# Performance work log

Measured on AMD Instinct MI355X. Metric: run time of the kernel, lower is better.

## Reference

```python
import jax, jax.numpy as jnp
import numpy as np

D = 2048          # input_size
B_NECK = 512      # bottleneck_size
NUM_LANGS = 16
ZETA = 1.1
GAMMA = -0.1
LN_EPS = 1e-5


def setup_inputs() -> dict:
    key = jax.random.key(0)
    ks = jax.random.split(key, 8)
    x = jax.random.normal(ks[0], (8, 2048, D), dtype=jnp.float32)
    # xavier_uniform for linear weights
    lim_d = float(np.sqrt(6.0 / (D + B_NECK)))
    down_w = jax.random.uniform(ks[1], (B_NECK, D), minval=-lim_d, maxval=lim_d, dtype=jnp.float32)
    up_w = jax.random.uniform(ks[2], (D, B_NECK), minval=-lim_d, maxval=lim_d, dtype=jnp.float32)
    down_b = jnp.zeros((B_NECK,), dtype=jnp.float32)
    up_b = jnp.zeros((D,), dtype=jnp.float32)
    ln_g = jnp.ones((D,), dtype=jnp.float32)
    ln_b = jnp.zeros((D,), dtype=jnp.float32)
    down_loga = 0.01 * jax.random.normal(ks[3], (NUM_LANGS, D), dtype=jnp.float32)
    up_loga = 0.01 * jax.random.normal(ks[4], (NUM_LANGS, B_NECK), dtype=jnp.float32)
    return {"x": x, "down_w": down_w, "down_b": down_b, "up_w": up_w,
            "up_b": up_b, "ln_g": ln_g, "ln_b": ln_b,
            "down_loga": down_loga, "up_loga": up_loga, "lang_id": 3}


def _det_mask(loga_row):
    # eval-mode L0 gate: hardtanh(sigmoid(loga)*(zeta-gamma)+gamma, 0, 1)
    return jnp.clip(jax.nn.sigmoid(loga_row) * (ZETA - GAMMA) + GAMMA, 0.0, 1.0)


def reference(x, down_w, down_b, up_w, up_b, ln_g, ln_b, down_loga, up_loga, lang_id):
    shortcut = x
    # LayerNorm over last dim
    mu = jnp.mean(x, axis=-1, keepdims=True)
    var = jnp.mean(jnp.square(x - mu), axis=-1, keepdims=True)
    h = (x - mu) * jax.lax.rsqrt(var + LN_EPS) * ln_g + ln_b
    # down projection with per-input-feature gate (mask scales weight columns)
    dmask = _det_mask(down_loga[lang_id])            # [D]
    h = jnp.einsum('bsd,kd->bsk', h * dmask, down_w) + down_b  # [B,S,B_NECK]
    h = jax.nn.relu(h)
    # up projection with per-bottleneck gate
    umask = _det_mask(up_loga[lang_id])              # [B_NECK]
    h = jnp.einsum('bsk,dk->bsd', h * umask, up_w) + up_b       # [B,S,D]
    return h + shortcut
```

## Files before the change

kernel.cpp:

```cpp
#include <hip/hip_runtime.h>
#include <cstdint>
#include <cstddef>

typedef unsigned short u16;
typedef __attribute__((ext_vector_type(4))) float f32x4;
typedef __attribute__((ext_vector_type(8))) short bf16x8;

#define LN_EPS 1e-5f

__device__ __forceinline__ u16 f2bf(float f) {
  unsigned int u = __float_as_uint(f);
  u += 0x7FFFu + ((u >> 16) & 1u);
  return (u16)(u >> 16);
}

__device__ __forceinline__ float l0gate(float loga) {
  float s = 1.0f / (1.0f + expf(-loga));
  float v = s * 1.2f - 0.1f;
  return fminf(fmaxf(v, 0.0f), 1.0f);
}

__device__ __forceinline__ void llds16(u16* lds, const u16* g) {
  __builtin_amdgcn_global_load_lds(
      (const __attribute__((address_space(1))) unsigned int*)g,
      (__attribute__((address_space(3))) unsigned int*)lds, 16, 0, 0);
}

__global__ __launch_bounds__(256) void prep_weights(
    const float* __restrict__ dw, const float* __restrict__ uw,
    const float* __restrict__ dloga, const float* __restrict__ uloga,
    const int* __restrict__ lang,
    u16* __restrict__ dwb, u16* __restrict__ uwb) {
  const int lid = lang[0];
  const unsigned i = blockIdx.x * 256u + threadIdx.x;
  dwb[i] = f2bf(dw[i] * l0gate(dloga[lid * 2048 + (i & 2047u)]));
  uwb[i] = f2bf(uw[i] * l0gate(uloga[lid * 512 + (i & 511u)]));
}

__global__ __launch_bounds__(256) void ln_kernel(
    const float* __restrict__ x, const float* __restrict__ g,
    const float* __restrict__ b, u16* __restrict__ h1) {
  const int row = blockIdx.x;
  const int tid = threadIdx.x;
  const float4* xr = (const float4*)(x + (size_t)row * 2048);
  float4 v0 = xr[tid * 2 + 0];
  float4 v1 = xr[tid * 2 + 1];
  float s = v0.x + v0.y + v0.z + v0.w + v1.x + v1.y + v1.z + v1.w;
  float q = v0.x * v0.x + v0.y * v0.y + v0.z * v0.z + v0.w * v0.w +
            v1.x * v1.x + v1.y * v1.y + v1.z * v1.z + v1.w * v1.w;
#pragma unroll
  for (int off = 32; off > 0; off >>= 1) {
    s += __shfl_down(s, off, 64);
    q += __shfl_down(q, off, 64);
  }
  __shared__ float ss[4], sq[4], sstat[2];
  const int wave = tid >> 6, lane = tid & 63;
  if (lane == 0) { ss[wave] = s; sq[wave] = q; }
  __syncthreads();
  if (tid == 0) {
    float S = ss[0] + ss[1] + ss[2] + ss[3];
    float Q = sq[0] + sq[1] + sq[2] + sq[3];
    float mu = S * (1.0f / 2048.0f);
    float var = Q * (1.0f / 2048.0f) - mu * mu;
    sstat[0] = mu;
    sstat[1] = rsqrtf(var + LN_EPS);
  }
  __syncthreads();
  const float mu = sstat[0], rs = sstat[1];
  const float4* g4 = (const float4*)g;
  const float4* b4 = (const float4*)b;
  float4 ga = g4[tid * 2], gb = g4[tid * 2 + 1];
  float4 ba = b4[tid * 2], bb = b4[tid * 2 + 1];
  union { u16 us[8]; uint4 u; } p;
  p.us[0] = f2bf((v0.x - mu) * rs * ga.x + ba.x);
  p.us[1] = f2bf((v0.y - mu) * rs * ga.y + ba.y);
  p.us[2] = f2bf((v0.z - mu) * rs * ga.z + ba.z);
  p.us[3] = f2bf((v0.w - mu) * rs * ga.w + ba.w);
  p.us[4] = f2bf((v1.x - mu) * rs * gb.x + bb.x);
  p.us[5] = f2bf((v1.y - mu) * rs * gb.y + bb.y);
  p.us[6] = f2bf((v1.z - mu) * rs * gb.z + bb.z);
  p.us[7] = f2bf((v1.w - mu) * rs * gb.w + bb.w);
  ((uint4*)(h1 + (size_t)row * 2048))[tid] = p.u;
}

template <int EPI>
__global__ __launch_bounds__(256) void gemm_bt(
    const u16* __restrict__ A, const u16* __restrict__ B,
    int M, int N, int K, int NX,
    const float* __restrict__ bias,
    const float* __restrict__ resid,
    void* __restrict__ outp) {
  __shared__ __align__(16) char smem[65536];
  u16* As = (u16*)smem;
  u16* Bs = (u16*)(smem + 32768);
  float* Cs = (float*)smem;

  const int tid = threadIdx.x;
  const int wave = tid >> 6, lane = tid & 63;
  const int wr = (wave >> 1) * 64;
  const int wc = (wave & 1) * 64;
  const int lrow = lane & 15, lk = lane >> 4;

  const int nwg = gridDim.x;
  const int wg = (blockIdx.x & 7) * (nwg >> 3) + (blockIdx.x >> 3);
  const int bx = wg % NX, by = wg / NX;
  const size_t m0 = (size_t)by * 128;
  const size_t n0 = (size_t)bx * 128;

  f32x4 acc[4][4] = {};

  const int srow = lane >> 3;
  const int sslot = (lane & 7) ^ ((lane >> 3) & 7);
  auto STAGE = [&](int buf, int k0) {
#pragma unroll
    for (int c = 0; c < 4; ++c) {
      const int seg = c * 4 + wave;
      const int r = seg * 8 + srow;
      llds16(As + buf * 8192 + seg * 512, A + (m0 + r) * (size_t)K + (k0 + sslot * 8));
      llds16(Bs + buf * 8192 + seg * 512, B + (n0 + r) * (size_t)K + (k0 + sslot * 8));
    }
  };

  const int NT = K >> 6;
  STAGE(0, 0);

  for (int t = 0; t < NT; ++t) {
    const int cur = t & 1;
    if (t + 1 < NT) {
      STAGE(cur ^ 1, (t + 1) << 6);
      asm volatile("s_waitcnt vmcnt(8)" ::: "memory");
    } else {
      asm volatile("s_waitcnt vmcnt(0)" ::: "memory");
    }
    __builtin_amdgcn_s_barrier();
    asm volatile("" ::: "memory");

    const u16* Ab = As + cur * 8192;
    const u16* Bb = Bs + cur * 8192;
#pragma unroll
    for (int ks = 0; ks < 2; ++ks) {
      bf16x8 af[4], bfr[4];
#pragma unroll
      for (int m = 0; m < 4; ++m)
        af[m] = *(const bf16x8*)&Ab[(wr + m * 16 + lrow) * 64 +
                                    ((unsigned)(ks * 4 + lk) ^ (lane & 7)) * 8];
#pragma unroll
      for (int n = 0; n < 4; ++n)
        bfr[n] = *(const bf16x8*)&Bb[(wc + n * 16 + lrow) * 64 +
                                     ((unsigned)(ks * 4 + lk) ^ (lane & 7)) * 8];
      __builtin_amdgcn_s_setprio(1);
#pragma unroll
      for (int m = 0; m < 4; ++m)
#pragma unroll
        for (int n = 0; n < 4; ++n)
          acc[m][n] = __builtin_amdgcn_mfma_f32_16x16x32_bf16(af[m], bfr[n],
                                                              acc[m][n], 0, 0, 0);
      __builtin_amdgcn_s_setprio(0);
    }
    asm volatile("s_waitcnt lgkmcnt(0)" ::: "memory");
    __builtin_amdgcn_s_barrier();
    asm volatile("" ::: "memory");
  }

  float4 rsd[16];
  if (EPI == 2) {
#pragma unroll
    for (int j = 0; j < 16; ++j) {
      const int flat = tid * 4 + j * 1024;
      const int row = flat >> 7, col = flat & 127;
      rsd[j] = *(const float4*)&resid[(m0 + row) * (size_t)N + n0 + col];
    }
  }

#pragma unroll
  for (int n = 0; n < 4; ++n) {
    const int col = wc + n * 16 + lrow;
    const float bv = bias[n0 + col];
#pragma unroll
    for (int m = 0; m < 4; ++m) {
#pragma unroll
      for (int r = 0; r < 4; ++r) {
        const int row = wr + m * 16 + lk * 4 + r;
        Cs[row * 128 + ((col + ((row >> 2) << 3)) & 127)] = acc[m][n][r] + bv;
      }
    }
  }
  asm volatile("s_waitcnt lgkmcnt(0)" ::: "memory");
  __builtin_amdgcn_s_barrier();
  asm volatile("" ::: "memory");

  if (EPI == 2) {
#pragma unroll
    for (int j = 0; j < 16; ++j) {
      const int flat = tid * 4 + j * 1024;
      const int row = flat >> 7, col = flat & 127;
      const float4 c = *(const float4*)&Cs[row * 128 + ((col + ((row >> 2) << 3)) & 127)];
      float4 o;
      o.x = c.x + rsd[j].x; o.y = c.y + rsd[j].y;
      o.z = c.z + rsd[j].z; o.w = c.w + rsd[j].w;
      *(float4*)&((float*)outp)[(m0 + row) * (size_t)N + n0 + col] = o;
    }
  } else {
#pragma unroll
    for (int j = 0; j < 8; ++j) {
      const int flat = tid * 8 + j * 2048;
      const int row = flat >> 7, col = flat & 127;
      const int cp = (col + ((row >> 2) << 3)) & 127;
      const float4 c0 = *(const float4*)&Cs[row * 128 + cp];
      const float4 c1 = *(const float4*)&Cs[row * 128 + cp + 4];
      union { u16 us[8]; uint4 u; } p;
      p.us[0] = f2bf(fmaxf(c0.x, 0.0f)); p.us[1] = f2bf(fmaxf(c0.y, 0.0f));
      p.us[2] = f2bf(fmaxf(c0.z, 0.0f)); p.us[3] = f2bf(fmaxf(c0.w, 0.0f));
      p.us[4] = f2bf(fmaxf(c1.x, 0.0f)); p.us[5] = f2bf(fmaxf(c1.y, 0.0f));
      p.us[6] = f2bf(fmaxf(c1.z, 0.0f)); p.us[7] = f2bf(fmaxf(c1.w, 0.0f));
      *(uint4*)&((u16*)outp)[(m0 + row) * (size_t)N + n0 + col] = p.u;
    }
  }
}

extern "C" void kernel_launch(void* const* d_in, const int* in_sizes, int n_in,
                              void* d_out, int out_size, void* d_ws, size_t ws_size,
                              hipStream_t stream) {
  const float* x         = (const float*)d_in[0];
  const float* down_w    = (const float*)d_in[1];
  const float* down_b    = (const float*)d_in[2];
  const float* up_w      = (const float*)d_in[3];
  const float* up_b      = (const float*)d_in[4];
  const float* ln_g      = (const float*)d_in[5];
  const float* ln_b      = (const float*)d_in[6];
  const float* down_loga = (const float*)d_in[7];
  const float* up_loga   = (const float*)d_in[8];
  const int*   lang      = (const int*)d_in[9];

  const int D = 2048, BNK = 512;
  const int M = in_sizes[0] / D;

  char* ws = (char*)d_ws;
  u16* h1  = (u16*)ws;
  u16* h2  = (u16*)(ws + (size_t)M * D * 2);
  u16* dwb = (u16*)(ws + (size_t)M * D * 2 + (size_t)M * BNK * 2);
  u16* uwb = dwb + (size_t)BNK * D;

  prep_weights<<<(BNK * D) / 256, 256, 0, stream>>>(down_w, up_w, down_loga,
                                                    up_loga, lang, dwb, uwb);
  ln_kernel<<<M, 256, 0, stream>>>(x, ln_g, ln_b, h1);
  const int nwg1 = (BNK / 128) * (M / 128);
  const int nwg2 = (D / 128) * (M / 128);
  gemm_bt<1><<<nwg1, 256, 0, stream>>>(h1, dwb, M, BNK, D, BNK / 128,
                                       down_b, nullptr, h2);
  gemm_bt<2><<<nwg2, 256, 0, stream>>>(h2, uwb, M, D, BNK, D / 128,
                                       up_b, x, d_out);
}
```

Before: 153.1 us.

## Shrink GEMM tiles to 128x64 with K-step 32 and raise occupancy

Changes the GEMM workgroup tile from 128x128 with a K-step of 64 to 128x64 with a K-step of 32. This halves shared memory to 32KB and requests 4 workgroups per CU through launch bounds, aiming for more occupancy and more workgroups across the CUs. The LDS XOR swizzle on the fragment reads is dropped, which may cause bank conflicts. Each tile also gets less reuse per load, and the shorter K-step doubles the number of barrier iterations.

```diff
diff --git a/kernel.cpp b/kernel.cpp
--- a/kernel.cpp
+++ b/kernel.cpp
@@ -84,104 +84,101 @@
 }
 
 template <int EPI>
-__global__ __launch_bounds__(256) void gemm_bt(
+__global__ __launch_bounds__(256, 4) void gemm_bt(
     const u16* __restrict__ A, const u16* __restrict__ B,
     int M, int N, int K, int NX,
     const float* __restrict__ bias,
     const float* __restrict__ resid,
     void* __restrict__ outp) {
-  __shared__ __align__(16) char smem[65536];
+  __shared__ __align__(16) char smem[32768];
   u16* As = (u16*)smem;
-  u16* Bs = (u16*)(smem + 32768);
+  u16* Bs = (u16*)(smem + 16384);
   float* Cs = (float*)smem;
 
   const int tid = threadIdx.x;
   const int wave = tid >> 6, lane = tid & 63;
   const int wr = (wave >> 1) * 64;
-  const int wc = (wave & 1) * 64;
+  const int wcc = (wave & 1) * 32;
   const int lrow = lane & 15, lk = lane >> 4;
 
   const int nwg = gridDim.x;
   const int wg = (blockIdx.x & 7) * (nwg >> 3) + (blockIdx.x >> 3);
   const int bx = wg % NX, by = wg / NX;
   const size_t m0 = (size_t)by * 128;
-  const size_t n0 = (size_t)bx * 128;
-
-  f32x4 acc[4][4] = {};
-
-  const int srow = lane >> 3;
-  const int sslot = (lane & 7) ^ ((lane >> 3) & 7);
+  const size_t n0 = (size_t)bx * 64;
+
+  f32x4 acc[4][2] = {};
+
+  const int crow = lane >> 2;
+  const int ckk = (lane & 3) * 8;
   auto STAGE = [&](int buf, int k0) {
 #pragma unroll
-    for (int c = 0; c < 4; ++c) {
-      const int seg = c * 4 + wave;
-      const int r = seg * 8 + srow;
-      llds16(As + buf * 8192 + seg * 512, A + (m0 + r) * (size_t)K + (k0 + sslot * 8));
-      llds16(Bs + buf * 8192 + seg * 512, B + (n0 + r) * (size_t)K + (k0 + sslot * 8));
-    }
+    for (int c = 0; c < 2; ++c) {
+      const int q = wave * 2 + c;
+      llds16(As + buf * 4096 + q * 512,
+             A + (m0 + q * 16 + crow) * (size_t)K + (k0 + ckk));
+    }
+    llds16(Bs + buf * 2048 + wave * 512,
+           B + (n0 + wave * 16 + crow) * (size_t)K + (k0 + ckk));
   };
 
-  const int NT = K >> 6;
+  const int NT = K >> 5;
   STAGE(0, 0);
 
   for (int t = 0; t < NT; ++t) {
     const int cur = t & 1;
     if (t + 1 < NT) {
-      STAGE(cur ^ 1, (t + 1) << 6);
-      asm volatile("s_waitcnt vmcnt(8)" ::: "memory");
+      STAGE(cur ^ 1, (t + 1) << 5);
+      asm volatile("s_waitcnt vmcnt(3)" ::: "memory");
     } else {
       asm volatile("s_waitcnt vmcnt(0)" ::: "memory");
     }
     __builtin_amdgcn_s_barrier();
     asm volatile("" ::: "memory");
 
-    const u16* Ab = As + cur * 8192;
-    const u16* Bb = Bs + cur * 8192;
-#pragma unroll
-    for (int ks = 0; ks < 2; ++ks) {
-      bf16x8 af[4], bfr[4];
-#pragma unroll
-      for (int m = 0; m < 4; ++m)
-        af[m] = *(const bf16x8*)&Ab[(wr + m * 16 + lrow) * 64 +
-                                    ((unsigned)(ks * 4 + lk) ^ (lane & 7)) * 8];
-#pragma unroll
-      for (int n = 0; n < 4; ++n)
-        bfr[n] = *(const bf16x8*)&Bb[(wc + n * 16 + lrow) * 64 +
-                                     ((unsigned)(ks * 4 + lk) ^ (lane & 7)) * 8];
-      __builtin_amdgcn_s_setprio(1);
-#pragma unroll
-      for (int m = 0; m < 4; ++m)
-#pragma unroll
-        for (int n = 0; n < 4; ++n)
-          acc[m][n] = __builtin_amdgcn_mfma_f32_16x16x32_bf16(af[m], bfr[n],
-                                                              acc[m][n], 0, 0, 0);
-      __builtin_amdgcn_s_setprio(0);
-    }
+    const u16* Ab = As + cur * 4096;
+    const u16* Bb = Bs + cur * 2048;
+    bf16x8 af[4], bfr[2];
+#pragma unroll
+    for (int m = 0; m < 4; ++m)
+      af[m] = *(const bf16x8*)&Ab[(wr + m * 16 + lrow) * 32 + lk * 8];
+#pragma unroll
+    for (int n = 0; n < 2; ++n)
+      bfr[n] = *(const bf16x8*)&Bb[(wcc + n * 16 + lrow) * 32 + lk * 8];
+    __builtin_amdgcn_s_setprio(1);
+#pragma unroll
+    for (int m = 0; m < 4; ++m)
+#pragma unroll
+      for (int n = 0; n < 2; ++n)
+        acc[m][n] = __builtin_amdgcn_mfma_f32_16x16x32_bf16(af[m], bfr[n],
+                                                            acc[m][n], 0, 0, 0);
+    __builtin_amdgcn_s_setprio(0);
+
     asm volatile("s_waitcnt lgkmcnt(0)" ::: "memory");
     __builtin_amdgcn_s_barrier();
     asm volatile("" ::: "memory");
   }
 
-  float4 rsd[16];
+  float4 rsd[8];
   if (EPI == 2) {
 #pragma unroll
-    for (int j = 0; j < 16; ++j) {
+    for (int j = 0; j < 8; ++j) {
       const int flat = tid * 4 + j * 1024;
-      const int row = flat >> 7, col = flat & 127;
-      rsd[j] = *(const float4*)&resid[(m0 + row) * (size_t)N + n0 + col];
-    }
-  }
-
-#pragma unroll
-  for (int n = 0; n < 4; ++n) {
-    const int col = wc + n * 16 + lrow;
-    const float bv = bias[n0 + col];
+      const int row = flat >> 6, c = flat & 63;
+      rsd[j] = *(const float4*)&resid[(m0 + row) * (size_t)N + n0 + c];
+    }
+  }
+
+#pragma unroll
+  for (int n = 0; n < 2; ++n) {
+    const int c = wcc + n * 16 + lrow;
+    const float bv = bias[n0 + c];
 #pragma unroll
     for (int m = 0; m < 4; ++m) {
 #pragma unroll
       for (int r = 0; r < 4; ++r) {
         const int row = wr + m * 16 + lk * 4 + r;
-        Cs[row * 128 + ((col + ((row >> 2) << 3)) & 127)] = acc[m][n][r] + bv;
+        Cs[row * 64 + ((c + ((row >> 2) << 3)) & 63)] = acc[m][n][r] + bv;
       }
     }
   }
@@ -191,29 +188,29 @@
 
   if (EPI == 2) {
 #pragma unroll
-    for (int j = 0; j < 16; ++j) {
+    for (int j = 0; j < 8; ++j) {
       const int flat = tid * 4 + j * 1024;
-      const int row = flat >> 7, col = flat & 127;
-      const float4 c = *(const float4*)&Cs[row * 128 + ((col + ((row >> 2) << 3)) & 127)];
+      const int row = flat >> 6, c = flat & 63;
+      const float4 cc = *(const float4*)&Cs[row * 64 + ((c + ((row >> 2) << 3)) & 63)];
       float4 o;
-      o.x = c.x + rsd[j].x; o.y = c.y + rsd[j].y;
-      o.z = c.z + rsd[j].z; o.w = c.w + rsd[j].w;
-      *(float4*)&((float*)outp)[(m0 + row) * (size_t)N + n0 + col] = o;
+      o.x = cc.x + rsd[j].x; o.y = cc.y + rsd[j].y;
+      o.z = cc.z + rsd[j].z; o.w = cc.w + rsd[j].w;
+      *(float4*)&((float*)outp)[(m0 + row) * (size_t)N + n0 + c] = o;
     }
   } else {
 #pragma unroll
-    for (int j = 0; j < 8; ++j) {
+    for (int j = 0; j < 4; ++j) {
       const int flat = tid * 8 + j * 2048;
-      const int row = flat >> 7, col = flat & 127;
-      const int cp = (col + ((row >> 2) << 3)) & 127;
-      const float4 c0 = *(const float4*)&Cs[row * 128 + cp];
-      const float4 c1 = *(const float4*)&Cs[row * 128 + cp + 4];
+      const int row = flat >> 6, c = flat & 63;
+      const int cp = (c + ((row >> 2) << 3)) & 63;
+      const float4 c0 = *(const float4*)&Cs[row * 64 + cp];
+      const float4 c1 = *(const float4*)&Cs[row * 64 + cp + 4];
       union { u16 us[8]; uint4 u; } p;
       p.us[0] = f2bf(fmaxf(c0.x, 0.0f)); p.us[1] = f2bf(fmaxf(c0.y, 0.0f));
       p.us[2] = f2bf(fmaxf(c0.z, 0.0f)); p.us[3] = f2bf(fmaxf(c0.w, 0.0f));
       p.us[4] = f2bf(fmaxf(c1.x, 0.0f)); p.us[5] = f2bf(fmaxf(c1.y, 0.0f));
       p.us[6] = f2bf(fmaxf(c1.z, 0.0f)); p.us[7] = f2bf(fmaxf(c1.w, 0.0f));
-      *(uint4*)&((u16*)outp)[(m0 + row) * (size_t)N + n0 + col] = p.u;
+      *(uint4*)&((u16*)outp)[(m0 + row) * (size_t)N + n0 + c] = p.u;
     }
   }
 }
@@ -244,10 +241,10 @@
   prep_weights<<<(BNK * D) / 256, 256, 0, stream>>>(down_w, up_w, down_loga,
                                                     up_loga, lang, dwb, uwb);
   ln_kernel<<<M, 256, 0, stream>>>(x, ln_g, ln_b, h1);
-  const int nwg1 = (BNK / 128) * (M / 128);
-  const int nwg2 = (D / 128) * (M / 128);
-  gemm_bt<1><<<nwg1, 256, 0, stream>>>(h1, dwb, M, BNK, D, BNK / 128,
+  const int nwg1 = (BNK / 64) * (M / 128);
+  const int nwg2 = (D / 64) * (M / 128);
+  gemm_bt<1><<<nwg1, 256, 0, stream>>>(h1, dwb, M, BNK, D, BNK / 64,
                                        down_b, nullptr, h2);
-  gemm_bt<2><<<nwg2, 256, 0, stream>>>(h2, uwb, M, D, BNK, D / 128,
+  gemm_bt<2><<<nwg2, 256, 0, stream>>>(h2, uwb, M, D, BNK, D / 64,
                                        up_b, x, d_out);
 }
```

New measurement: 180.1 us. 17.6% more time.

## Fold LayerNorm into down-projection GEMM via algebraic mean/scale correction

Applied to the files above, without the earlier changes.

Removes the separate LayerNorm kernel and its bf16 intermediate. The down GEMM now reads raw fp32 x, converts it to bf16 in registers while accumulating per-row sums and sums of squares, and applies the normalisation in the epilogue as rs*(acc - mu*u) + w. The gain is folded into the weights, and a new prep kernel computes u and w from the weights, beta and bias. The up GEMM also prefetches the residual during its K loop. The risk is precision, since un-normalised x is rounded to bf16 and the mean is subtracted after accumulation, which can cause cancellation. Each down-GEMM block also rereads x, once per output column tile.

```diff
diff --git a/kernel.cpp b/kernel.cpp
--- a/kernel.cpp
+++ b/kernel.cpp
@@ -29,111 +29,112 @@
 __global__ __launch_bounds__(256) void prep_weights(
     const float* __restrict__ dw, const float* __restrict__ uw,
     const float* __restrict__ dloga, const float* __restrict__ uloga,
-    const int* __restrict__ lang,
+    const int* __restrict__ lang, const float* __restrict__ g,
     u16* __restrict__ dwb, u16* __restrict__ uwb) {
   const int lid = lang[0];
   const unsigned i = blockIdx.x * 256u + threadIdx.x;
-  dwb[i] = f2bf(dw[i] * l0gate(dloga[lid * 2048 + (i & 2047u)]));
+  dwb[i] = f2bf(dw[i] * l0gate(dloga[lid * 2048 + (i & 2047u)]) * g[i & 2047u]);
   uwb[i] = f2bf(uw[i] * l0gate(uloga[lid * 512 + (i & 511u)]));
 }
 
-__global__ __launch_bounds__(256) void ln_kernel(
-    const float* __restrict__ x, const float* __restrict__ g,
-    const float* __restrict__ b, u16* __restrict__ h1) {
-  const int row = blockIdx.x;
-  const int tid = threadIdx.x;
-  const float4* xr = (const float4*)(x + (size_t)row * 2048);
-  float4 v0 = xr[tid * 2 + 0];
-  float4 v1 = xr[tid * 2 + 1];
-  float s = v0.x + v0.y + v0.z + v0.w + v1.x + v1.y + v1.z + v1.w;
-  float q = v0.x * v0.x + v0.y * v0.y + v0.z * v0.z + v0.w * v0.w +
-            v1.x * v1.x + v1.y * v1.y + v1.z * v1.z + v1.w * v1.w;
+__global__ __launch_bounds__(256) void prep_uv(
+    const float* __restrict__ dw, const float* __restrict__ dloga,
+    const int* __restrict__ lang, const float* __restrict__ g,
+    const float* __restrict__ lnb, const float* __restrict__ down_b,
+    float* __restrict__ u, float* __restrict__ wv) {
+  const int lid = lang[0];
+  const int n = blockIdx.x * 4 + (threadIdx.x >> 6);
+  const int lane = threadIdx.x & 63;
+  float su = 0.0f, sv = 0.0f;
+  for (int d = lane; d < 2048; d += 64) {
+    const float w = dw[n * 2048 + d] * l0gate(dloga[lid * 2048 + d]);
+    su += w * g[d];
+    sv += w * lnb[d];
+  }
 #pragma unroll
   for (int off = 32; off > 0; off >>= 1) {
-    s += __shfl_down(s, off, 64);
-    q += __shfl_down(q, off, 64);
-  }
-  __shared__ float ss[4], sq[4], sstat[2];
-  const int wave = tid >> 6, lane = tid & 63;
-  if (lane == 0) { ss[wave] = s; sq[wave] = q; }
-  __syncthreads();
-  if (tid == 0) {
-    float S = ss[0] + ss[1] + ss[2] + ss[3];
-    float Q = sq[0] + sq[1] + sq[2] + sq[3];
-    float mu = S * (1.0f / 2048.0f);
-    float var = Q * (1.0f / 2048.0f) - mu * mu;
-    sstat[0] = mu;
-    sstat[1] = rsqrtf(var + LN_EPS);
-  }
-  __syncthreads();
-  const float mu = sstat[0], rs = sstat[1];
-  const float4* g4 = (const float4*)g;
-  const float4* b4 = (const float4*)b;
-  float4 ga = g4[tid * 2], gb = g4[tid * 2 + 1];
-  float4 ba = b4[tid * 2], bb = b4[tid * 2 + 1];
-  union { u16 us[8]; uint4 u; } p;
-  p.us[0] = f2bf((v0.x - mu) * rs * ga.x + ba.x);
-  p.us[1] = f2bf((v0.y - mu) * rs * ga.y + ba.y);
-  p.us[2] = f2bf((v0.z - mu) * rs * ga.z + ba.z);
-  p.us[3] = f2bf((v0.w - mu) * rs * ga.w + ba.w);
-  p.us[4] = f2bf((v1.x - mu) * rs * gb.x + bb.x);
-  p.us[5] = f2bf((v1.y - mu) * rs * gb.y + bb.y);
-  p.us[6] = f2bf((v1.z - mu) * rs * gb.z + bb.z);
-  p.us[7] = f2bf((v1.w - mu) * rs * gb.w + bb.w);
-  ((uint4*)(h1 + (size_t)row * 2048))[tid] = p.u;
-}
-
-template <int EPI>
-__global__ __launch_bounds__(256) void gemm_bt(
-    const u16* __restrict__ A, const u16* __restrict__ B,
-    int M, int N, int K, int NX,
-    const float* __restrict__ bias,
-    const float* __restrict__ resid,
-    void* __restrict__ outp) {
+    su += __shfl_down(su, off, 64);
+    sv += __shfl_down(sv, off, 64);
+  }
+  if (lane == 0) { u[n] = su; wv[n] = sv + down_b[n]; }
+}
+
+__global__ __launch_bounds__(256) void gemm1_ln(
+    const float* __restrict__ X, const u16* __restrict__ Bw,
+    int M, const float* __restrict__ uu, const float* __restrict__ wvv,
+    u16* __restrict__ h2out) {
+  const int K = 2048;
   __shared__ __align__(16) char smem[65536];
   u16* As = (u16*)smem;
   u16* Bs = (u16*)(smem + 32768);
   float* Cs = (float*)smem;
+  __shared__ float stats[128][2];
 
   const int tid = threadIdx.x;
   const int wave = tid >> 6, lane = tid & 63;
-  const int wr = (wave >> 1) * 64;
-  const int wc = (wave & 1) * 64;
+  const int wr = (wave >> 1) * 64, wc = (wave & 1) * 64;
   const int lrow = lane & 15, lk = lane >> 4;
 
   const int nwg = gridDim.x;
   const int wg = (blockIdx.x & 7) * (nwg >> 3) + (blockIdx.x >> 3);
-  const int bx = wg % NX, by = wg / NX;
-  const size_t m0 = (size_t)by * 128;
-  const size_t n0 = (size_t)bx * 128;
+  const int bx = wg & 3, by = wg >> 2;
+  const size_t m0 = (size_t)by * 128, n0 = (size_t)bx * 128;
 
   f32x4 acc[4][4] = {};
-
-  const int srow = lane >> 3;
-  const int sslot = (lane & 7) ^ ((lane >> 3) & 7);
-  auto STAGE = [&](int buf, int k0) {
+  float sx[4] = {0.f, 0.f, 0.f, 0.f}, qx[4] = {0.f, 0.f, 0.f, 0.f};
+
+  const int arow = tid >> 3;
+  const int acol = ((tid & 7) ^ ((tid >> 3) & 7)) * 8;
+  const int brow = lane >> 3;
+  const int bsrc = ((lane & 7) ^ ((lane >> 3) & 7)) * 8;
+
+  f32x4 xa[4][2];
+  auto A_ISSUE = [&](int k0) {
+#pragma unroll
+    for (int j = 0; j < 4; ++j) {
+      const float* p = X + (m0 + arow + 32 * j) * (size_t)K + k0 + acol;
+      xa[j][0] = *(const f32x4*)p;
+      xa[j][1] = *(const f32x4*)(p + 4);
+    }
+  };
+  auto B_ISSUE = [&](int buf, int k0) {
 #pragma unroll
     for (int c = 0; c < 4; ++c) {
       const int seg = c * 4 + wave;
-      const int r = seg * 8 + srow;
-      llds16(As + buf * 8192 + seg * 512, A + (m0 + r) * (size_t)K + (k0 + sslot * 8));
-      llds16(Bs + buf * 8192 + seg * 512, B + (n0 + r) * (size_t)K + (k0 + sslot * 8));
-    }
-  };
-
-  const int NT = K >> 6;
-  STAGE(0, 0);
+      llds16(Bs + buf * 8192 + seg * 512,
+             Bw + (n0 + seg * 8 + brow) * (size_t)K + k0 + bsrc);
+    }
+  };
+  auto A_WRITE = [&](int buf) {
+#pragma unroll
+    for (int j = 0; j < 4; ++j) {
+      union { u16 us[8]; uint4 u4; } p;
+#pragma unroll
+      for (int e = 0; e < 4; ++e) {
+        const float v0 = xa[j][0][e], v1 = xa[j][1][e];
+        sx[j] += v0 + v1;
+        qx[j] += v0 * v0 + v1 * v1;
+        p.us[e] = f2bf(v0);
+        p.us[4 + e] = f2bf(v1);
+      }
+      *(uint4*)(As + buf * 8192 + (tid + 256 * j) * 8) = p.u4;
+    }
+  };
+
+  const int NT = K / 64;
+  A_ISSUE(0);
+  B_ISSUE(0, 0);
+  asm volatile("s_waitcnt vmcnt(4)" ::: "memory");
+  A_WRITE(0);
+  asm volatile("s_waitcnt vmcnt(0)" ::: "memory");
+  asm volatile("s_waitcnt lgkmcnt(0)" ::: "memory");
+  __builtin_amdgcn_s_barrier();
+  asm volatile("" ::: "memory");
 
   for (int t = 0; t < NT; ++t) {
     const int cur = t & 1;
-    if (t + 1 < NT) {
-      STAGE(cur ^ 1, (t + 1) << 6);
-      asm volatile("s_waitcnt vmcnt(8)" ::: "memory");
-    } else {
-      asm volatile("s_waitcnt vmcnt(0)" ::: "memory");
-    }
-    __builtin_amdgcn_s_barrier();
-    asm volatile("" ::: "memory");
+    const bool more = (t + 1 < NT);
+    if (more) { A_ISSUE((t + 1) * 64); B_ISSUE(cur ^ 1, (t + 1) * 64); }
 
     const u16* Ab = As + cur * 8192;
     const u16* Bb = Bs + cur * 8192;
@@ -143,11 +144,11 @@
 #pragma unroll
       for (int m = 0; m < 4; ++m)
         af[m] = *(const bf16x8*)&Ab[(wr + m * 16 + lrow) * 64 +
-                                    ((unsigned)(ks * 4 + lk) ^ (lane & 7)) * 8];
+                                    ((unsigned)((ks * 4 + lk) ^ (lane & 7))) * 8];
 #pragma unroll
       for (int n = 0; n < 4; ++n)
         bfr[n] = *(const bf16x8*)&Bb[(wc + n * 16 + lrow) * 64 +
-                                     ((unsigned)(ks * 4 + lk) ^ (lane & 7)) * 8];
+                                     ((unsigned)((ks * 4 + lk) ^ (lane & 7))) * 8];
       __builtin_amdgcn_s_setprio(1);
 #pragma unroll
       for (int m = 0; m < 4; ++m)
@@ -157,64 +158,188 @@
                                                               acc[m][n], 0, 0, 0);
       __builtin_amdgcn_s_setprio(0);
     }
+    if (more) {
+      asm volatile("s_waitcnt vmcnt(4)" ::: "memory");
+      A_WRITE(cur ^ 1);
+      asm volatile("s_waitcnt vmcnt(0)" ::: "memory");
+    }
     asm volatile("s_waitcnt lgkmcnt(0)" ::: "memory");
     __builtin_amdgcn_s_barrier();
     asm volatile("" ::: "memory");
   }
 
-  float4 rsd[16];
-  if (EPI == 2) {
-#pragma unroll
-    for (int j = 0; j < 16; ++j) {
-      const int flat = tid * 4 + j * 1024;
-      const int row = flat >> 7, col = flat & 127;
-      rsd[j] = *(const float4*)&resid[(m0 + row) * (size_t)N + n0 + col];
-    }
-  }
-
+  float ucol[4], wcol[4];
 #pragma unroll
   for (int n = 0; n < 4; ++n) {
-    const int col = wc + n * 16 + lrow;
-    const float bv = bias[n0 + col];
-#pragma unroll
-    for (int m = 0; m < 4; ++m) {
-#pragma unroll
-      for (int r = 0; r < 4; ++r) {
-        const int row = wr + m * 16 + lk * 4 + r;
-        Cs[row * 128 + ((col + ((row >> 2) << 3)) & 127)] = acc[m][n][r] + bv;
-      }
+    const int c = wc + n * 16 + lrow;
+    ucol[n] = uu[n0 + c];
+    wcol[n] = wvv[n0 + c];
+  }
+#pragma unroll
+  for (int j = 0; j < 4; ++j) {
+#pragma unroll
+    for (int off = 1; off < 8; off <<= 1) {
+      sx[j] += __shfl_xor(sx[j], off, 64);
+      qx[j] += __shfl_xor(qx[j], off, 64);
+    }
+  }
+  if ((lane & 7) == 0) {
+#pragma unroll
+    for (int j = 0; j < 4; ++j) {
+      const int r = (tid >> 3) + 32 * j;
+      const float mu = sx[j] * (1.0f / 2048.0f);
+      const float var = qx[j] * (1.0f / 2048.0f) - mu * mu;
+      stats[r][0] = mu;
+      stats[r][1] = rsqrtf(var + LN_EPS);
     }
   }
   asm volatile("s_waitcnt lgkmcnt(0)" ::: "memory");
   __builtin_amdgcn_s_barrier();
   asm volatile("" ::: "memory");
 
-  if (EPI == 2) {
-#pragma unroll
-    for (int j = 0; j < 16; ++j) {
-      const int flat = tid * 4 + j * 1024;
-      const int row = flat >> 7, col = flat & 127;
-      const float4 c = *(const float4*)&Cs[row * 128 + ((col + ((row >> 2) << 3)) & 127)];
-      float4 o;
-      o.x = c.x + rsd[j].x; o.y = c.y + rsd[j].y;
-      o.z = c.z + rsd[j].z; o.w = c.w + rsd[j].w;
-      *(float4*)&((float*)outp)[(m0 + row) * (size_t)N + n0 + col] = o;
-    }
-  } else {
-#pragma unroll
-    for (int j = 0; j < 8; ++j) {
-      const int flat = tid * 8 + j * 2048;
-      const int row = flat >> 7, col = flat & 127;
-      const int cp = (col + ((row >> 2) << 3)) & 127;
-      const float4 c0 = *(const float4*)&Cs[row * 128 + cp];
-      const float4 c1 = *(const float4*)&Cs[row * 128 + cp + 4];
-      union { u16 us[8]; uint4 u; } p;
-      p.us[0] = f2bf(fmaxf(c0.x, 0.0f)); p.us[1] = f2bf(fmaxf(c0.y, 0.0f));
-      p.us[2] = f2bf(fmaxf(c0.z, 0.0f)); p.us[3] = f2bf(fmaxf(c0.w, 0.0f));
-      p.us[4] = f2bf(fmaxf(c1.x, 0.0f)); p.us[5] = f2bf(fmaxf(c1.y, 0.0f));
-      p.us[6] = f2bf(fmaxf(c1.z, 0.0f)); p.us[7] = f2bf(fmaxf(c1.w, 0.0f));
-      *(uint4*)&((u16*)outp)[(m0 + row) * (size_t)N + n0 + col] = p.u;
-    }
+#pragma unroll
+  for (int m = 0; m < 4; ++m) {
+#pragma unroll
+    for (int r = 0; r < 4; ++r) {
+      const int row = wr + m * 16 + lk * 4 + r;
+      const float mu = stats[row][0], rs = stats[row][1];
+#pragma unroll
+      for (int n = 0; n < 4; ++n) {
+        const int c = wc + n * 16 + lrow;
+        const float val = rs * (acc[m][n][r] - mu * ucol[n]) + wcol[n];
+        Cs[row * 128 + ((c + ((row >> 2) << 3)) & 127)] = val;
+      }
+    }
+  }
+  asm volatile("s_waitcnt lgkmcnt(0)" ::: "memory");
+  __builtin_amdgcn_s_barrier();
+  asm volatile("" ::: "memory");
+
+#pragma unroll
+  for (int j = 0; j < 8; ++j) {
+    const int flat = tid * 8 + j * 2048;
+    const int row = flat >> 7, c = flat & 127;
+    const int cp = (c + ((row >> 2) << 3)) & 127;
+    const f32x4 c0 = *(const f32x4*)&Cs[row * 128 + cp];
+    const f32x4 c1 = *(const f32x4*)&Cs[row * 128 + cp + 4];
+    union { u16 us[8]; uint4 u; } p;
+    p.us[0] = f2bf(fmaxf(c0[0], 0.0f)); p.us[1] = f2bf(fmaxf(c0[1], 0.0f));
+    p.us[2] = f2bf(fmaxf(c0[2], 0.0f)); p.us[3] = f2bf(fmaxf(c0[3], 0.0f));
+    p.us[4] = f2bf(fmaxf(c1[0], 0.0f)); p.us[5] = f2bf(fmaxf(c1[1], 0.0f));
+    p.us[6] = f2bf(fmaxf(c1[2], 0.0f)); p.us[7] = f2bf(fmaxf(c1[3], 0.0f));
+    *(uint4*)&h2out[(m0 + row) * 512 + n0 + c] = p.u;
+  }
+}
+
+__global__ __launch_bounds__(256) void gemm2(
+    const u16* __restrict__ A, const u16* __restrict__ Bw,
+    int M, const float* __restrict__ bias,
+    const float* __restrict__ resid, float* __restrict__ outp) {
+  const int K = 512, N = 2048;
+  __shared__ __align__(16) char smem[65536];
+  u16* As = (u16*)smem;
+  u16* Bs = (u16*)(smem + 32768);
+  float* Cs = (float*)smem;
+
+  const int tid = threadIdx.x;
+  const int wave = tid >> 6, lane = tid & 63;
+  const int wr = (wave >> 1) * 64, wc = (wave & 1) * 64;
+  const int lrow = lane & 15, lk = lane >> 4;
+
+  const int nwg = gridDim.x;
+  const int wg = (blockIdx.x & 7) * (nwg >> 3) + (blockIdx.x >> 3);
+  const int bx = wg & 15, by = wg >> 4;
+  const size_t m0 = (size_t)by * 128, n0 = (size_t)bx * 128;
+
+  f32x4 acc[4][4] = {};
+
+  const int srow = lane >> 3;
+  const int sslot = ((lane & 7) ^ ((lane >> 3) & 7)) * 8;
+  auto STAGE = [&](int buf, int k0) {
+#pragma unroll
+    for (int c = 0; c < 4; ++c) {
+      const int seg = c * 4 + wave;
+      const int r = seg * 8 + srow;
+      llds16(As + buf * 8192 + seg * 512, A + (m0 + r) * (size_t)K + (k0 + sslot));
+      llds16(Bs + buf * 8192 + seg * 512, Bw + (n0 + r) * (size_t)K + (k0 + sslot));
+    }
+  };
+
+  f32x4 rsd[16];
+  auto RSD = [&](int j) {
+    const int flat = tid * 4 + j * 1024;
+    const int row = flat >> 7, c = flat & 127;
+    rsd[j] = *(const f32x4*)&resid[(m0 + row) * (size_t)N + n0 + c];
+  };
+
+  STAGE(0, 0);
+#pragma unroll
+  for (int t = 0; t < 8; ++t) {
+    const int cur = t & 1;
+    if (t < 7) {
+      STAGE(cur ^ 1, (t + 1) * 64);
+      RSD(2 * t); RSD(2 * t + 1);
+      asm volatile("s_waitcnt vmcnt(10)" ::: "memory");
+    } else {
+      RSD(14); RSD(15);
+      asm volatile("s_waitcnt vmcnt(4)" ::: "memory");
+    }
+    __builtin_amdgcn_s_barrier();
+    asm volatile("" ::: "memory");
+
+    const u16* Ab = As + cur * 8192;
+    const u16* Bb = Bs + cur * 8192;
+#pragma unroll
+    for (int ks = 0; ks < 2; ++ks) {
+      bf16x8 af[4], bfr[4];
+#pragma unroll
+      for (int m = 0; m < 4; ++m)
+        af[m] = *(const bf16x8*)&Ab[(wr + m * 16 + lrow) * 64 +
+                                    ((unsigned)((ks * 4 + lk) ^ (lane & 7))) * 8];
+#pragma unroll
+      for (int n = 0; n < 4; ++n)
+        bfr[n] = *(const bf16x8*)&Bb[(wc + n * 16 + lrow) * 64 +
+                                     ((unsigned)((ks * 4 + lk) ^ (lane & 7))) * 8];
+      __builtin_amdgcn_s_setprio(1);
+#pragma unroll
+      for (int m = 0; m < 4; ++m)
+#pragma unroll
+        for (int n = 0; n < 4; ++n)
+          acc[m][n] = __builtin_amdgcn_mfma_f32_16x16x32_bf16(af[m], bfr[n],
+                                                              acc[m][n], 0, 0, 0);
+      __builtin_amdgcn_s_setprio(0);
+    }
+    asm volatile("s_waitcnt lgkmcnt(0)" ::: "memory");
+    __builtin_amdgcn_s_barrier();
+    asm volatile("" ::: "memory");
+  }
+
+#pragma unroll
+  for (int n = 0; n < 4; ++n) {
+    const int c = wc + n * 16 + lrow;
+    const float bv = bias[n0 + c];
+#pragma unroll
+    for (int m = 0; m < 4; ++m) {
+#pragma unroll
+      for (int r = 0; r < 4; ++r) {
+        const int row = wr + m * 16 + lk * 4 + r;
+        Cs[row * 128 + ((c + ((row >> 2) << 3)) & 127)] = acc[m][n][r] + bv;
+      }
+    }
+  }
+  asm volatile("s_waitcnt lgkmcnt(0)" ::: "memory");
+  __builtin_amdgcn_s_barrier();
+  asm volatile("" ::: "memory");
+
+#pragma unroll
+  for (int j = 0; j < 16; ++j) {
+    const int flat = tid * 4 + j * 1024;
+    const int row = flat >> 7, c = flat & 127;
+    const f32x4 cc = *(const f32x4*)&Cs[row * 128 + ((c + ((row >> 2) << 3)) & 127)];
+    f32x4 o;
+    o[0] = cc[0] + rsd[j][0]; o[1] = cc[1] + rsd[j][1];
+    o[2] = cc[2] + rsd[j][2]; o[3] = cc[3] + rsd[j][3];
+    *(f32x4*)&outp[(m0 + row) * (size_t)N + n0 + c] = o;
   }
 }
 
@@ -236,18 +361,17 @@
   const int M = in_sizes[0] / D;
 
   char* ws = (char*)d_ws;
-  u16* h1  = (u16*)ws;
-  u16* h2  = (u16*)(ws + (size_t)M * D * 2);
-  u16* dwb = (u16*)(ws + (size_t)M * D * 2 + (size_t)M * BNK * 2);
-  u16* uwb = dwb + (size_t)BNK * D;
+  u16*   h2  = (u16*)ws;
+  u16*   dwb = (u16*)(ws + (size_t)M * BNK * 2);
+  u16*   uwb = dwb + (size_t)BNK * D;
+  float* u_  = (float*)(uwb + (size_t)D * BNK);
+  float* wv_ = u_ + BNK;
 
   prep_weights<<<(BNK * D) / 256, 256, 0, stream>>>(down_w, up_w, down_loga,
-                                                    up_loga, lang, dwb, uwb);
-  ln_kernel<<<M, 256, 0, stream>>>(x, ln_g, ln_b, h1);
-  const int nwg1 = (BNK / 128) * (M / 128);
-  const int nwg2 = (D / 128) * (M / 128);
-  gemm_bt<1><<<nwg1, 256, 0, stream>>>(h1, dwb, M, BNK, D, BNK / 128,
-                                       down_b, nullptr, h2);
-  gemm_bt<2><<<nwg2, 256, 0, stream>>>(h2, uwb, M, D, BNK, D / 128,
-                                       up_b, x, d_out);
-}
+                                                    up_loga, lang, ln_g, dwb, uwb);
+  prep_uv<<<BNK / 4, 256, 0, stream>>>(down_w, down_loga, lang, ln_g, ln_b,
+                                       down_b, u_, wv_);
+  gemm1_ln<<<(M / 128) * (BNK / 128), 256, 0, stream>>>(x, dwb, M, u_, wv_, h2);
+  gemm2<<<(M / 128) * (D / 128), 256, 0, stream>>>(h2, uwb, M, up_b, x,
+                                                   (float*)d_out);
+}
```

After: 160.7 us. 4.9% more time.
